# Kernel tuning notes

Measured on AMD Instinct MI355X. Metric: run time of the kernel, lower is better.

Reference implementation:

```python
import jax, jax.numpy as jnp
import numpy as np

B, S, IN_F, OUT_F, RANK = 4, 4096, 4096, 4096, 64

def soft_threshold24(w):
    # 2:4 soft-threshold pruning: groups of 4 along last dim; keep top-2 |w|,
    # soft-threshold by t = 3rd-largest |w| in each group: sign(w)*relu(|w|-t).
    g = w.reshape(w.shape[0], -1, 4)
    a = jnp.abs(g)
    t = jnp.sort(a, axis=-1)[..., 1:2]  # 3rd largest = 2nd smallest of 4
    s = jnp.sign(g) * jnp.maximum(a - t, 0.0)
    return s.reshape(w.shape)

def fake_fp8_mm(a, b):
    # simulated fp8 GEMM per fake_fp8_mm: fp16 operands, fp32 accumulate/output
    return jnp.matmul(a.astype(jnp.float16), b.astype(jnp.float16),
                      preferred_element_type=jnp.float32)

def setup_inputs():
    key = jax.random.key(0)
    k1, k2, k3 = jax.random.split(key, 3)
    x = jax.random.normal(k1, (B, S, IN_F), jnp.float32)
    std_a = float(np.sqrt(2.0 / (IN_F + RANK)))   # xavier_normal_
    std_b = float(np.sqrt(2.0 / (OUT_F + RANK)))
    weight_A = jax.random.normal(k2, (IN_F, RANK), jnp.float32) * std_a
    weight_B = jax.random.normal(k3, (OUT_F, RANK), jnp.float32) * std_b
    bias = jnp.zeros((OUT_F,), jnp.float32)
    scale_A = jnp.float32(1.0)
    scale_B = jnp.float32(1.0)
    return {"x": x, "weight_A": weight_A, "weight_B": weight_B,
            "bias": bias, "scale_A": scale_A, "scale_B": scale_B}

def reference(x, weight_A, weight_B, bias, scale_A, scale_B):
    wA = soft_threshold24(weight_A) * scale_A      # [IN, R], 2:4 sparse along R
    wB = soft_threshold24(weight_B) * scale_B      # [OUT, R], 2:4 sparse along R
    xf = x.reshape(-1, x.shape[-1])                # [N, IN]
    x_proj = fake_fp8_mm(xf, wA)                   # [N, R]   == FP8SparseOp(x, wA.T, None)
    out = fake_fp8_mm(x_proj, wB.T) + bias         # [N, OUT] == FP8SparseOp(x_proj, wB, bias)
    return out.reshape(*x.shape[:-1], OUT_F)
```

## Files before the change

kernel.cpp:

```cpp
#include <hip/hip_runtime.h>
#include <hip/hip_cooperative_groups.h>

namespace cg = cooperative_groups;

#define IN_FEAT 4096
#define OUT_FEAT 4096
#define RANK 64
#define NROWS 16384
#define TM 32
#define BT 512
#define NB 256
#define KC2 256
#define SXS 264
#define BR 256
#define BC 256
#define BS 72
#define KC 256
#define WA_STRIDE 264
#define XP_STRIDE 72

typedef _Float16 half_t;
typedef _Float16 f16x4 __attribute__((ext_vector_type(4)));
typedef _Float16 f16x8 __attribute__((ext_vector_type(8)));
typedef float f32x4 __attribute__((ext_vector_type(4)));

__device__ __forceinline__ f16x4 thr4(float4 v, float s) {
    float a0 = fabsf(v.x), a1 = fabsf(v.y), a2 = fabsf(v.z), a3 = fabsf(v.w);
    float lo1 = fminf(a0, a1), hi1 = fmaxf(a0, a1);
    float lo2 = fminf(a2, a3), hi2 = fmaxf(a2, a3);
    float t = fminf(fmaxf(lo1, lo2), fminf(hi1, hi2));
    f16x4 r;
    r[0] = (half_t)(copysignf(fmaxf(a0 - t, 0.0f), v.x) * s);
    r[1] = (half_t)(copysignf(fmaxf(a1 - t, 0.0f), v.y) * s);
    r[2] = (half_t)(copysignf(fmaxf(a2 - t, 0.0f), v.z) * s);
    r[3] = (half_t)(copysignf(fmaxf(a3 - t, 0.0f), v.w) * s);
    return r;
}

__device__ __forceinline__ f16x4 cvt4(f32x4 v) {
    f16x4 h;
    h[0] = (half_t)v[0]; h[1] = (half_t)v[1];
    h[2] = (half_t)v[2]; h[3] = (half_t)v[3];
    return h;
}

__global__ __launch_bounds__(BT) void coop_v3(
    const float* __restrict__ x, const float* __restrict__ wA,
    const float* __restrict__ wB, const float* __restrict__ bias,
    const float* __restrict__ scaleA, const float* __restrict__ scaleB,
    float* __restrict__ out, half_t* __restrict__ wAT, half_t* __restrict__ wBh,
    half_t* __restrict__ xpw)
{
    __shared__ __align__(16) char pool[BR * BS * 2 + BC * BS * 2];
    __shared__ __align__(16) float biasl[BC];

    int tid = threadIdx.x;
    int bid = blockIdx.x;

    {
        int id = bid * BT + tid;
        if (id < 65536) {
            int row = id >> 4;
            int gq  = id & 15;
            float s = scaleB[0];
            f16x4 h = thr4(*(const float4*)(wB + (size_t)row * RANK + gq * 4), s);
            *(f16x4*)(wBh + (size_t)row * RANK + gq * 4) = h;
        } else if (id < 65536 + 8192) {
            int t2 = id - 65536;
            int c4 = t2 & 15;
            int k8 = t2 >> 4;
            float s = scaleA[0];
            f16x8 vc0, vc1, vc2, vc3;
#pragma unroll
            for (int i = 0; i < 8; ++i) {
                float4 v = *(const float4*)(wA + (size_t)(k8 * 8 + i) * RANK + c4 * 4);
                f16x4 h = thr4(v, s);
                vc0[i] = h[0]; vc1[i] = h[1]; vc2[i] = h[2]; vc3[i] = h[3];
            }
            *(f16x8*)(wAT + (size_t)(c4 * 4 + 0) * IN_FEAT + k8 * 8) = vc0;
            *(f16x8*)(wAT + (size_t)(c4 * 4 + 1) * IN_FEAT + k8 * 8) = vc1;
            *(f16x8*)(wAT + (size_t)(c4 * 4 + 2) * IN_FEAT + k8 * 8) = vc2;
            *(f16x8*)(wAT + (size_t)(c4 * 4 + 3) * IN_FEAT + k8 * 8) = vc3;
        }
    }
    cg::this_grid().sync();

    int wave = tid >> 6;
    int lane = tid & 63;
    int l16  = lane & 15;
    int g    = lane >> 4;

    {
        half_t (*xs)[TM][SXS] = (half_t(*)[TM][SXS])pool;
        int stripe = wave & 1;
        int quad   = wave >> 1;
        int srow = tid >> 4;
        int sseg = tid & 15;

        for (int sub = 0; sub < 2; ++sub) {
            int rowbase = bid * (2 * TM) + sub * TM;
            const float* srcrow = x + (size_t)(rowbase + srow) * IN_FEAT + sseg * 4;

            {
                const f32x4* p = (const f32x4*)(srcrow);
                f32x4 a0 = p[0], a1 = p[16], a2 = p[32], a3 = p[48];
                half_t* dst = &xs[0][srow][sseg * 4];
                *(f16x4*)(dst +   0) = cvt4(a0);
                *(f16x4*)(dst +  64) = cvt4(a1);
                *(f16x4*)(dst + 128) = cvt4(a2);
                *(f16x4*)(dst + 192) = cvt4(a3);
            }
            __syncthreads();

            f32x4 acc = {0, 0, 0, 0};
            const half_t* wcol = wAT + (size_t)(quad * 16 + l16) * IN_FEAT;
            const half_t* arow = &xs[0][stripe * 16 + l16][0];
            const int xsstep = TM * SXS;
            f32x4 ld0, ld1, ld2, ld3;

            for (int c = 0; c < IN_FEAT / KC2; ++c) {
                f16x8 bfr[8];
#pragma unroll
                for (int j = 0; j < 8; ++j)
                    bfr[j] = *(const f16x8*)(wcol + c * KC2 + j * 32 + 8 * g);
                __builtin_amdgcn_sched_barrier(0);
                if (c + 1 < IN_FEAT / KC2) {
                    const f32x4* p = (const f32x4*)(srcrow + (c + 1) * KC2);
                    ld0 = p[0]; ld1 = p[16]; ld2 = p[32]; ld3 = p[48];
                }
                __builtin_amdgcn_sched_barrier(0);

                const half_t* ar = arow + (c & 1) * xsstep;
#pragma unroll
                for (int j = 0; j < 8; ++j) {
                    f16x8 a = *(const f16x8*)(ar + j * 32 + 8 * g);
                    acc = __builtin_amdgcn_mfma_f32_16x16x32_f16(a, bfr[j], acc, 0, 0, 0);
                }
                if (c + 1 < IN_FEAT / KC2) {
                    half_t* dst = &xs[(c + 1) & 1][srow][sseg * 4];
                    *(f16x4*)(dst +   0) = cvt4(ld0);
                    *(f16x4*)(dst +  64) = cvt4(ld1);
                    *(f16x4*)(dst + 128) = cvt4(ld2);
                    *(f16x4*)(dst + 192) = cvt4(ld3);
                }
                __syncthreads();
            }

#pragma unroll
            for (int r = 0; r < 4; ++r)
                xpw[(size_t)(rowbase + stripe * 16 + 4 * g + r) * RANK + quad * 16 + l16]
                    = (half_t)acc[r];
            __syncthreads();
        }
    }
    cg::this_grid().sync();

    {
        half_t (*xps)[BS] = (half_t(*)[BS])pool;
        half_t (*wbs)[BS] = (half_t(*)[BS])(pool + BR * BS * 2);

        int rb = (bid >> 2) * BR;

        {
            int row = tid >> 1, h = tid & 1;
            const half_t* src = xpw + (size_t)(rb + row) * RANK + h * 32;
            f16x8 v0 = *(const f16x8*)(src + 0);
            f16x8 v1 = *(const f16x8*)(src + 8);
            f16x8 v2 = *(const f16x8*)(src + 16);
            f16x8 v3 = *(const f16x8*)(src + 24);
            half_t* dst = &xps[row][h * 32];
            *(f16x8*)(dst + 0)  = v0;
            *(f16x8*)(dst + 8)  = v1;
            *(f16x8*)(dst + 16) = v2;
            *(f16x8*)(dst + 24) = v3;
        }

        int wrow = (wave & 1) * 128;
        int wcol = (wave >> 1) * 64;

        for (int t = 0; t < 4; ++t) {
            int cb = ((bid & 3) * 4 + t) * BC;

            {
                int col = tid >> 1, h = tid & 1;
                const half_t* src = wBh + (size_t)(cb + col) * RANK + h * 32;
                f16x8 v0 = *(const f16x8*)(src + 0);
                f16x8 v1 = *(const f16x8*)(src + 8);
                f16x8 v2 = *(const f16x8*)(src + 16);
                f16x8 v3 = *(const f16x8*)(src + 24);
                half_t* dst = &wbs[col][h * 32];
                *(f16x8*)(dst + 0)  = v0;
                *(f16x8*)(dst + 8)  = v1;
                *(f16x8*)(dst + 16) = v2;
                *(f16x8*)(dst + 24) = v3;
                if (tid < BC) biasl[tid] = bias[cb + tid];
            }
            __syncthreads();

            f16x8 bf0[4], bf1[4];
            f32x4 bv4[4];
#pragma unroll
            for (int ci = 0; ci < 4; ++ci) {
                int c16 = wcol + ci * 16 + l16;
                bf0[ci] = *(const f16x8*)&wbs[c16][8 * g];
                bf1[ci] = *(const f16x8*)&wbs[c16][32 + 8 * g];
                bv4[ci] = *(const f32x4*)&biasl[wcol + ci * 16 + 4 * g];
            }

            for (int rt = 0; rt < 8; ++rt) {
                const half_t* ar = &xps[wrow + rt * 16 + l16][0];
                f16x8 a0 = *(const f16x8*)(ar + 8 * g);
                f16x8 a1 = *(const f16x8*)(ar + 32 + 8 * g);
                size_t rowoff = (size_t)(rb + wrow + rt * 16 + l16) * OUT_FEAT;
#pragma unroll
                for (int ci = 0; ci < 4; ++ci) {
                    f32x4 acc2 = {0, 0, 0, 0};
                    acc2 = __builtin_amdgcn_mfma_f32_16x16x32_f16(bf0[ci], a0, acc2, 0, 0, 0);
                    acc2 = __builtin_amdgcn_mfma_f32_16x16x32_f16(bf1[ci], a1, acc2, 0, 0, 0);
                    f32x4 st;
                    st[0] = acc2[0] + bv4[ci][0];
                    st[1] = acc2[1] + bv4[ci][1];
                    st[2] = acc2[2] + bv4[ci][2];
                    st[3] = acc2[3] + bv4[ci][3];
                    int col0 = cb + wcol + ci * 16 + 4 * g;
                    *(f32x4*)&out[rowoff + col0] = st;
                }
            }
            __syncthreads();
        }
    }
}

__global__ __launch_bounds__(256) void fused_kernel(
    const float* __restrict__ x, const float* __restrict__ wA,
    const float* __restrict__ wB, const float* __restrict__ bias,
    const float* __restrict__ scaleA, const float* __restrict__ scaleB,
    float* __restrict__ out)
{
    __shared__ __align__(16) half_t wAsT[RANK][WA_STRIDE];
    __shared__ float xp_part[2][TM][XP_STRIDE];
    __shared__ __align__(16) half_t xp[TM][XP_STRIDE];

    int tid  = threadIdx.x;
    int wave = tid >> 6;
    int lane = tid & 63;
    int l16  = lane & 15;
    int g    = lane >> 4;
    int rowbase = blockIdx.x * TM;
    int stripe  = wave & 1;
    int ks      = wave >> 1;

    float sA = scaleA[0];
    float sB = scaleB[0];

    const float* xrow = x + (size_t)(rowbase + stripe * 16 + l16) * IN_FEAT;
    f32x4 acc[4] = {f32x4{0,0,0,0}, f32x4{0,0,0,0}, f32x4{0,0,0,0}, f32x4{0,0,0,0}};

    for (int chunk = 0; chunk < IN_FEAT / KC; ++chunk) {
        int k0 = chunk * KC;
#pragma unroll
        for (int pp = 0; pp < 2; ++pp) {
            int p = tid + pp * 256;
            int q = p & 15;
            int r = p >> 4;
            f16x8 vc0, vc1, vc2, vc3;
#pragma unroll
            for (int i = 0; i < 8; ++i) {
                float4 v = *(const float4*)(wA + (size_t)(k0 + 8 * r + i) * RANK + 4 * q);
                f16x4 h = thr4(v, sA);
                vc0[i] = h[0]; vc1[i] = h[1]; vc2[i] = h[2]; vc3[i] = h[3];
            }
            *(f16x8*)&wAsT[4 * q + 0][8 * r] = vc0;
            *(f16x8*)&wAsT[4 * q + 1][8 * r] = vc1;
            *(f16x8*)&wAsT[4 * q + 2][8 * r] = vc2;
            *(f16x8*)&wAsT[4 * q + 3][8 * r] = vc3;
        }
        __syncthreads();

#pragma unroll
        for (int it = 0; it < 4; ++it) {
            int kloc = ks * 128 + it * 32;
            float4 xa = *(const float4*)(xrow + k0 + kloc + 8 * g);
            float4 xb = *(const float4*)(xrow + k0 + kloc + 8 * g + 4);
            f16x8 a;
            a[0] = (half_t)xa.x; a[1] = (half_t)xa.y; a[2] = (half_t)xa.z; a[3] = (half_t)xa.w;
            a[4] = (half_t)xb.x; a[5] = (half_t)xb.y; a[6] = (half_t)xb.z; a[7] = (half_t)xb.w;
#pragma unroll
            for (int f = 0; f < 4; ++f) {
                f16x8 b = *(const f16x8*)&wAsT[16 * f + l16][kloc + 8 * g];
                acc[f] = __builtin_amdgcn_mfma_f32_16x16x32_f16(a, b, acc[f], 0, 0, 0);
            }
        }
        __syncthreads();
    }

#pragma unroll
    for (int f = 0; f < 4; ++f)
#pragma unroll
        for (int r = 0; r < 4; ++r)
            xp_part[ks][stripe * 16 + 4 * g + r][16 * f + l16] = acc[f][r];
    __syncthreads();

#pragma unroll
    for (int i = 0; i < (TM * RANK) / 256; ++i) {
        int e = i * 256 + tid;
        int r = e >> 6, c = e & 63;
        xp[r][c] = (half_t)(xp_part[0][r][c] + xp_part[1][r][c]);
    }
    __syncthreads();

    {
        const half_t* xprow = &xp[stripe * 16 + l16][0];
        f16x8 a0 = *(const f16x8*)(xprow + 8 * g);
        f16x8 a1 = *(const f16x8*)(xprow + 32 + 8 * g);

        int cb0 = ks * (OUT_FEAT / 2);
        for (int cb = cb0; cb < cb0 + OUT_FEAT / 2; cb += 16) {
            int col = cb + l16;
            const float* wp = wB + (size_t)col * RANK;
            float4 w00 = *(const float4*)(wp + 8 * g);
            float4 w01 = *(const float4*)(wp + 8 * g + 4);
            float4 w10 = *(const float4*)(wp + 32 + 8 * g);
            float4 w11 = *(const float4*)(wp + 32 + 8 * g + 4);
            f16x4 b00 = thr4(w00, sB), b01 = thr4(w01, sB);
            f16x4 b10 = thr4(w10, sB), b11 = thr4(w11, sB);
            f16x8 b0, b1;
            b0[0]=b00[0]; b0[1]=b00[1]; b0[2]=b00[2]; b0[3]=b00[3];
            b0[4]=b01[0]; b0[5]=b01[1]; b0[6]=b01[2]; b0[7]=b01[3];
            b1[0]=b10[0]; b1[1]=b10[1]; b1[2]=b10[2]; b1[3]=b10[3];
            b1[4]=b11[0]; b1[5]=b11[1]; b1[6]=b11[2]; b1[7]=b11[3];

            f32x4 acc2 = {0, 0, 0, 0};
            acc2 = __builtin_amdgcn_mfma_f32_16x16x32_f16(a0, b0, acc2, 0, 0, 0);
            acc2 = __builtin_amdgcn_mfma_f32_16x16x32_f16(a1, b1, acc2, 0, 0, 0);
            float bv = bias[col];
#pragma unroll
            for (int r = 0; r < 4; ++r)
                out[(size_t)(rowbase + stripe * 16 + 4 * g + r) * OUT_FEAT + col] = acc2[r] + bv;
        }
    }
}

extern "C" void kernel_launch(void* const* d_in, const int* in_sizes, int n_in,
                              void* d_out, int out_size, void* d_ws, size_t ws_size,
                              hipStream_t stream) {
    const float* x      = (const float*)d_in[0];
    const float* wA     = (const float*)d_in[1];
    const float* wB     = (const float*)d_in[2];
    const float* bias   = (const float*)d_in[3];
    const float* scaleA = (const float*)d_in[4];
    const float* scaleB = (const float*)d_in[5];
    float* out = (float*)d_out;

    const size_t WS_V3 = (size_t)RANK * IN_FEAT * 2
                       + (size_t)OUT_FEAT * RANK * 2
                       + (size_t)NROWS * RANK * 2;

    bool launched = false;
    if (ws_size >= WS_V3 && d_ws != nullptr) {
        half_t* wAT = (half_t*)d_ws;
        half_t* wBh = wAT + (size_t)RANK * IN_FEAT;
        half_t* xpw = wBh + (size_t)OUT_FEAT * RANK;
        void* args[] = {(void*)&x, (void*)&wA, (void*)&wB, (void*)&bias,
                        (void*)&scaleA, (void*)&scaleB, (void*)&out,
                        (void*)&wAT, (void*)&wBh, (void*)&xpw};
        hipError_t err = hipLaunchCooperativeKernel((void*)coop_v3,
                                                    dim3(NB), dim3(BT),
                                                    args, 0, stream);
        launched = (err == hipSuccess);
    }
    if (!launched) {
        fused_kernel<<<NROWS / TM, 256, 0, stream>>>(x, wA, wB, bias, scaleA, scaleB, out);
    }
}
```

Before: 218.5 us.

## Double block size to 1024 threads, running both row sub-tiles concurrently

The block size goes from 512 to 1024 threads. In the first GEMM, the two 32-row sub-tiles each block owns are now handled at the same time by two halves of the block, each with its own double-buffered shared-memory region, instead of in a serial loop. The second GEMM splits the 256x256 output tile across 16 waves, so each wave handles 4 row tiles instead of 8. The aim is more waves per CU to hide latency and shorter serial phases. The cost is twice the shared memory for the x staging buffers and fewer registers per thread under the larger launch bound, which could cause spills or make the cooperative launch fail and drop to the slow fallback kernel.

Result: slower. 226.3 us (+3.6%).

```diff
diff --git a/kernel.cpp b/kernel.cpp
--- a/kernel.cpp
+++ b/kernel.cpp
@@ -8,7 +8,7 @@
 #define RANK 64
 #define NROWS 16384
 #define TM 32
-#define BT 512
+#define BT 1024
 #define NB 256
 #define KC2 256
 #define SXS 264
@@ -44,7 +44,7 @@
     return h;
 }
 
-__global__ __launch_bounds__(BT) void coop_v3(
+__global__ __launch_bounds__(BT) void coop_v5(
     const float* __restrict__ x, const float* __restrict__ wA,
     const float* __restrict__ wB, const float* __restrict__ bias,
     const float* __restrict__ scaleA, const float* __restrict__ scaleB,
@@ -91,67 +91,66 @@
     int g    = lane >> 4;
 
     {
-        half_t (*xs)[TM][SXS] = (half_t(*)[TM][SXS])pool;
-        int stripe = wave & 1;
-        int quad   = wave >> 1;
-        int srow = tid >> 4;
-        int sseg = tid & 15;
-
-        for (int sub = 0; sub < 2; ++sub) {
-            int rowbase = bid * (2 * TM) + sub * TM;
-            const float* srcrow = x + (size_t)(rowbase + srow) * IN_FEAT + sseg * 4;
-
-            {
-                const f32x4* p = (const f32x4*)(srcrow);
-                f32x4 a0 = p[0], a1 = p[16], a2 = p[32], a3 = p[48];
-                half_t* dst = &xs[0][srow][sseg * 4];
-                *(f16x4*)(dst +   0) = cvt4(a0);
-                *(f16x4*)(dst +  64) = cvt4(a1);
-                *(f16x4*)(dst + 128) = cvt4(a2);
-                *(f16x4*)(dst + 192) = cvt4(a3);
+        half_t (*xs)[2][TM][SXS] = (half_t(*)[2][TM][SXS])pool;
+        int sub    = wave >> 3;
+        int w8     = wave & 7;
+        int stripe = w8 & 1;
+        int quad   = w8 >> 1;
+        int st     = tid & 511;
+        int srow   = st >> 4;
+        int sseg   = st & 15;
+        int rowbase = bid * 64 + sub * TM;
+        const float* srcrow = x + (size_t)(rowbase + srow) * IN_FEAT + sseg * 4;
+
+        {
+            const f32x4* p = (const f32x4*)(srcrow);
+            f32x4 a0 = p[0], a1 = p[16], a2 = p[32], a3 = p[48];
+            half_t* dst = &xs[sub][0][srow][sseg * 4];
+            *(f16x4*)(dst +   0) = cvt4(a0);
+            *(f16x4*)(dst +  64) = cvt4(a1);
+            *(f16x4*)(dst + 128) = cvt4(a2);
+            *(f16x4*)(dst + 192) = cvt4(a3);
+        }
+        __syncthreads();
+
+        f32x4 acc = {0, 0, 0, 0};
+        const half_t* wcol = wAT + (size_t)(quad * 16 + l16) * IN_FEAT;
+        const half_t* arow = &xs[sub][0][stripe * 16 + l16][0];
+        const int xsstep = TM * SXS;
+        f32x4 ld0, ld1, ld2, ld3;
+
+        for (int c = 0; c < IN_FEAT / KC2; ++c) {
+            f16x8 bfr[8];
+#pragma unroll
+            for (int j = 0; j < 8; ++j)
+                bfr[j] = *(const f16x8*)(wcol + c * KC2 + j * 32 + 8 * g);
+            __builtin_amdgcn_sched_barrier(0);
+            if (c + 1 < IN_FEAT / KC2) {
+                const f32x4* p = (const f32x4*)(srcrow + (c + 1) * KC2);
+                ld0 = p[0]; ld1 = p[16]; ld2 = p[32]; ld3 = p[48];
+            }
+            __builtin_amdgcn_sched_barrier(0);
+
+            const half_t* ar = arow + (c & 1) * xsstep;
+#pragma unroll
+            for (int j = 0; j < 8; ++j) {
+                f16x8 a = *(const f16x8*)(ar + j * 32 + 8 * g);
+                acc = __builtin_amdgcn_mfma_f32_16x16x32_f16(a, bfr[j], acc, 0, 0, 0);
+            }
+            if (c + 1 < IN_FEAT / KC2) {
+                half_t* dst = &xs[sub][(c + 1) & 1][srow][sseg * 4];
+                *(f16x4*)(dst +   0) = cvt4(ld0);
+                *(f16x4*)(dst +  64) = cvt4(ld1);
+                *(f16x4*)(dst + 128) = cvt4(ld2);
+                *(f16x4*)(dst + 192) = cvt4(ld3);
             }
             __syncthreads();
-
-            f32x4 acc = {0, 0, 0, 0};
-            const half_t* wcol = wAT + (size_t)(quad * 16 + l16) * IN_FEAT;
-            const half_t* arow = &xs[0][stripe * 16 + l16][0];
-            const int xsstep = TM * SXS;
-            f32x4 ld0, ld1, ld2, ld3;
-
-            for (int c = 0; c < IN_FEAT / KC2; ++c) {
-                f16x8 bfr[8];
-#pragma unroll
-                for (int j = 0; j < 8; ++j)
-                    bfr[j] = *(const f16x8*)(wcol + c * KC2 + j * 32 + 8 * g);
-                __builtin_amdgcn_sched_barrier(0);
-                if (c + 1 < IN_FEAT / KC2) {
-                    const f32x4* p = (const f32x4*)(srcrow + (c + 1) * KC2);
-                    ld0 = p[0]; ld1 = p[16]; ld2 = p[32]; ld3 = p[48];
-                }
-                __builtin_amdgcn_sched_barrier(0);
-
-                const half_t* ar = arow + (c & 1) * xsstep;
-#pragma unroll
-                for (int j = 0; j < 8; ++j) {
-                    f16x8 a = *(const f16x8*)(ar + j * 32 + 8 * g);
-                    acc = __builtin_amdgcn_mfma_f32_16x16x32_f16(a, bfr[j], acc, 0, 0, 0);
-                }
-                if (c + 1 < IN_FEAT / KC2) {
-                    half_t* dst = &xs[(c + 1) & 1][srow][sseg * 4];
-                    *(f16x4*)(dst +   0) = cvt4(ld0);
-                    *(f16x4*)(dst +  64) = cvt4(ld1);
-                    *(f16x4*)(dst + 128) = cvt4(ld2);
-                    *(f16x4*)(dst + 192) = cvt4(ld3);
-                }
-                __syncthreads();
-            }
-
-#pragma unroll
-            for (int r = 0; r < 4; ++r)
-                xpw[(size_t)(rowbase + stripe * 16 + 4 * g + r) * RANK + quad * 16 + l16]
-                    = (half_t)acc[r];
-            __syncthreads();
-        }
+        }
+
+#pragma unroll
+        for (int r = 0; r < 4; ++r)
+            xpw[(size_t)(rowbase + stripe * 16 + 4 * g + r) * RANK + quad * 16 + l16]
+                = (half_t)acc[r];
     }
     cg::this_grid().sync();
 
@@ -162,37 +161,29 @@
         int rb = (bid >> 2) * BR;
 
         {
-            int row = tid >> 1, h = tid & 1;
-            const half_t* src = xpw + (size_t)(rb + row) * RANK + h * 32;
+            int row = tid >> 2, q4 = tid & 3;
+            const half_t* src = xpw + (size_t)(rb + row) * RANK + q4 * 16;
             f16x8 v0 = *(const f16x8*)(src + 0);
             f16x8 v1 = *(const f16x8*)(src + 8);
-            f16x8 v2 = *(const f16x8*)(src + 16);
-            f16x8 v3 = *(const f16x8*)(src + 24);
-            half_t* dst = &xps[row][h * 32];
-            *(f16x8*)(dst + 0)  = v0;
-            *(f16x8*)(dst + 8)  = v1;
-            *(f16x8*)(dst + 16) = v2;
-            *(f16x8*)(dst + 24) = v3;
-        }
-
-        int wrow = (wave & 1) * 128;
-        int wcol = (wave >> 1) * 64;
+            half_t* dst = &xps[row][q4 * 16];
+            *(f16x8*)(dst + 0) = v0;
+            *(f16x8*)(dst + 8) = v1;
+        }
+
+        int wrow = (wave & 3) * 64;
+        int wcol = (wave >> 2) * 64;
 
         for (int t = 0; t < 4; ++t) {
             int cb = ((bid & 3) * 4 + t) * BC;
 
             {
-                int col = tid >> 1, h = tid & 1;
-                const half_t* src = wBh + (size_t)(cb + col) * RANK + h * 32;
+                int row = tid >> 2, q4 = tid & 3;
+                const half_t* src = wBh + (size_t)(cb + row) * RANK + q4 * 16;
                 f16x8 v0 = *(const f16x8*)(src + 0);
                 f16x8 v1 = *(const f16x8*)(src + 8);
-                f16x8 v2 = *(const f16x8*)(src + 16);
-                f16x8 v3 = *(const f16x8*)(src + 24);
-                half_t* dst = &wbs[col][h * 32];
-                *(f16x8*)(dst + 0)  = v0;
-                *(f16x8*)(dst + 8)  = v1;
-                *(f16x8*)(dst + 16) = v2;
-                *(f16x8*)(dst + 24) = v3;
+                half_t* dst = &wbs[row][q4 * 16];
+                *(f16x8*)(dst + 0) = v0;
+                *(f16x8*)(dst + 8) = v1;
                 if (tid < BC) biasl[tid] = bias[cb + tid];
             }
             __syncthreads();
@@ -207,7 +198,7 @@
                 bv4[ci] = *(const f32x4*)&biasl[wcol + ci * 16 + 4 * g];
             }
 
-            for (int rt = 0; rt < 8; ++rt) {
+            for (int rt = 0; rt < 4; ++rt) {
                 const half_t* ar = &xps[wrow + rt * 16 + l16][0];
                 f16x8 a0 = *(const f16x8*)(ar + 8 * g);
                 f16x8 a1 = *(const f16x8*)(ar + 32 + 8 * g);
@@ -352,19 +343,19 @@
     const float* scaleB = (const float*)d_in[5];
     float* out = (float*)d_out;
 
-    const size_t WS_V3 = (size_t)RANK * IN_FEAT * 2
+    const size_t WS_V5 = (size_t)RANK * IN_FEAT * 2
                        + (size_t)OUT_FEAT * RANK * 2
                        + (size_t)NROWS * RANK * 2;
 
     bool launched = false;
-    if (ws_size >= WS_V3 && d_ws != nullptr) {
+    if (ws_size >= WS_V5 && d_ws != nullptr) {
         half_t* wAT = (half_t*)d_ws;
         half_t* wBh = wAT + (size_t)RANK * IN_FEAT;
         half_t* xpw = wBh + (size_t)OUT_FEAT * RANK;
         void* args[] = {(void*)&x, (void*)&wA, (void*)&wB, (void*)&bias,
                         (void*)&scaleA, (void*)&scaleB, (void*)&out,
                         (void*)&wAT, (void*)&wBh, (void*)&xpw};
-        hipError_t err = hipLaunchCooperativeKernel((void*)coop_v3,
+        hipError_t err = hipLaunchCooperativeKernel((void*)coop_v5,
                                                     dim3(NB), dim3(BT),
                                                     args, 0, stream);
         launched = (err == hipSuccess);
```
